# Optimization experiments

Hardware: AMD Instinct MI355X
Metric: run time of the kernel (lower is better)

## Reference

```python
import jax, jax.numpy as jnp
import numpy as np

H, HD, NKV = 16, 128, 4           # heads, head_dim, n_kv_heads (kv_groups=4)
SEL_TOPK, SEL_DIM, SEL_HEADS = 64, 64, 1
ROPE_BASE = 10000.0


def _rope_emb(t, hd):
    inv = 1.0 / (ROPE_BASE ** (jnp.arange(0, hd, 2, dtype=jnp.float32) / hd))
    freqs = jnp.arange(t, dtype=jnp.float32)[:, None] * inv[None, :]
    return jnp.concatenate([freqs, freqs], axis=-1)  # [t, hd]


def _apply_rotary(x, rope):
    # x: [b, t, h, hd]; rope: [t, hd] (rot_dim == hd here)
    cos = jnp.cos(rope)[None, :, None, :]
    sin = jnp.sin(rope)[None, :, None, :]
    x1, x2 = x[..., ::2], x[..., 1::2]
    c, s = cos[..., ::2], sin[..., ::2]
    rot = jnp.stack([x1 * c - x2 * s, x1 * s + x2 * c], axis=-1)
    return rot.reshape(x.shape)


def _selector_mask(q, k):
    # q, k: [b, H, t, hd] in UNrotated form (selector_rope='none'); causal=True
    b, h, t, d = q.shape
    qs = q[:, :SEL_HEADS, :, :SEL_DIM]
    ks = k[:, :SEL_HEADS, :, :SEL_DIM]
    scores = jnp.einsum('bhqd,bhkd->bhqk', qs, ks) / np.sqrt(SEL_DIM).astype(np.float32)
    future = jnp.triu(jnp.ones((t, t), bool), 1)
    scores = jnp.where(future[None, None], -jnp.inf, scores)
    idx = jax.lax.top_k(scores, SEL_TOPK)[1]  # [b, h_sel, t, keep]
    rows = jnp.arange(t)
    scatter_row = lambda im: jnp.zeros((t, t), bool).at[rows[:, None], im].set(True)
    sel = jax.vmap(jax.vmap(scatter_row))(idx)          # [b, h_sel, t, t]
    sel = sel.at[:, :, rows, rows].set(True)            # diagonal always kept
    sel = sel & jnp.tril(jnp.ones((t, t), bool))[None, None]
    sel = jnp.any(sel, axis=1, keepdims=True)           # h_sel < h -> broadcast mask
    return jnp.where(sel, 0.0, -jnp.inf).astype(jnp.float32)


def reference(x, Wq, bq, Wkd, bkd, Wku, bku, Wo, bo):
    b, t, d = x.shape
    G = H // NKV
    q = (x @ Wq + bq).reshape(b, t, H, HD)
    kv = (x @ Wkd + bkd) @ Wku + bku                    # MLA: down then up projection
    k = kv[..., : NKV * HD].reshape(b, t, NKV, HD)
    v = kv[..., NKV * HD:].reshape(b, t, NKV, HD)
    rope = _rope_emb(t, HD)
    qb = _apply_rotary(q, rope).transpose(0, 2, 1, 3)                     # [b,H,t,hd]
    kb = jnp.repeat(_apply_rotary(k, rope).transpose(0, 2, 1, 3), G, 1)   # GQA expand
    vb = jnp.repeat(v.transpose(0, 2, 1, 3), G, 1)
    # selector mask from unrotated q/k, detached (selector_detach=True)
    qu = jax.lax.stop_gradient(q.transpose(0, 2, 1, 3))
    ku = jnp.repeat(jax.lax.stop_gradient(k.transpose(0, 2, 1, 3)), G, 1)
    mask = _selector_mask(qu, ku)                                         # [b,1,t,t]
    scores = jnp.einsum('bhqd,bhkd->bhqk', qb, kb) / np.sqrt(HD).astype(np.float32)
    attn = jax.nn.softmax(scores + mask, axis=-1)
    y = jnp.einsum('bhqk,bhkd->bhqd', attn, vb)
    y = y.transpose(0, 2, 1, 3).reshape(b, t, H * HD)
    return y @ Wo + bo


def setup_inputs() -> dict:
    key = jax.random.key(0)
    ks = jax.random.split(key, 6)
    B, T, D, LAT = 2, 2048, 2048, 512
    s = 0.02
    return {
        'x': jax.random.normal(ks[0], (B, T, D), jnp.float32),
        'Wq': jax.random.normal(ks[1], (D, H * HD), jnp.float32) * s,
        'bq': jnp.zeros((H * HD,), jnp.float32),
        'Wkd': jax.random.normal(ks[2], (D, LAT), jnp.float32) * s,
        'bkd': jnp.zeros((LAT,), jnp.float32),
        'Wku': jax.random.normal(ks[3], (LAT, 2 * NKV * HD), jnp.float32) * s,
        'bku': jnp.zeros((2 * NKV * HD,), jnp.float32),
        'Wo': jax.random.normal(ks[4], (H * HD, D), jnp.float32) * s,
        'bo': jnp.zeros((D,), jnp.float32),
    }
```

## Files before the change

kernel.cpp:

```cpp
#include <hip/hip_runtime.h>

typedef unsigned int u32;
typedef unsigned long long u64;
typedef _Float16 f16;
typedef __attribute__((ext_vector_type(2))) _Float16 f16x2;
typedef __attribute__((ext_vector_type(4))) _Float16 f16x4;
typedef __attribute__((ext_vector_type(8))) _Float16 f16x8;
typedef __attribute__((ext_vector_type(4))) float f32x4;
typedef __attribute__((ext_vector_type(2))) double f64x2;


__device__ __forceinline__ int suX(int jj) { return jj ^ ((jj >> 4) & 7); }

__device__ __forceinline__ void dev_transpose_cast(char* smem, int bx, int by,
                                                   const float* __restrict__ in,
                                                   f16* __restrict__ out, int R, int C)
{
  float* tile = (float*)smem;
  int c0 = bx * 32, r0 = by * 32;
  int tx = threadIdx.x & 31, ty = threadIdx.x >> 5;
  #pragma unroll
  for (int i = ty; i < 32; i += 8) tile[i * 33 + tx] = in[(size_t)(r0 + i) * C + c0 + tx];
  __syncthreads();
  #pragma unroll
  for (int i = ty; i < 32; i += 8) out[(size_t)(c0 + i) * R + r0 + tx] = (f16)tile[tx * 33 + i];
}

__global__ __launch_bounds__(256) void k_megaP(const float* __restrict__ Wq, f16* __restrict__ WqT,
                                               const float* __restrict__ Wkd, f16* __restrict__ WkdT,
                                               const float* __restrict__ Wku, f16* __restrict__ WkuT,
                                               const float* __restrict__ Wo, f16* __restrict__ WoT,
                                               const float* __restrict__ x, f16* __restrict__ xh,
                                               double* __restrict__ Bsel,
                                               const float* __restrict__ bq,
                                               const float* __restrict__ bkd,
                                               const float* __restrict__ bku,
                                               double* __restrict__ bsel,
                                               float* __restrict__ rc, float* __restrict__ rs)
{
  __shared__ __align__(16) char smem[4224];
  const int id = blockIdx.x;
  const int tid = threadIdx.x;
  if (id < 4096) {
    dev_transpose_cast(smem, id & 63, id >> 6, Wq, WqT, 2048, 2048);
  } else if (id < 5120) {
    int g = id - 4096;
    dev_transpose_cast(smem, g & 15, g >> 4, Wkd, WkdT, 2048, 512);
  } else if (id < 5632) {
    int g = id - 5120;
    dev_transpose_cast(smem, g & 31, g >> 5, Wku, WkuT, 512, 1024);
  } else if (id < 9728) {
    int g = id - 5632;
    dev_transpose_cast(smem, g & 63, g >> 6, Wo, WoT, 2048, 2048);
  } else if (id < 17920) {
    int i = (id - 9728) * 256 + tid;
    f32x4 v = *(const f32x4*)&x[(size_t)i * 4];
    f16x4 h; h.x = (f16)v.x; h.y = (f16)v.y; h.z = (f16)v.z; h.w = (f16)v.w;
    *(f16x4*)&xh[(size_t)i * 4] = h;
  } else if (id < 18432) {
    const int k = (id - 17920) * 4 + (tid >> 6);
    const int j = tid & 63;
    Bsel[(size_t)k * 128 + j] = (double)Wq[(size_t)k * 2048 + j];
    double s = 0.0;
    for (int l = 0; l < 512; ++l)
      s = fma((double)Wkd[(size_t)k * 512 + l], (double)Wku[(size_t)l * 1024 + j], s);
    Bsel[(size_t)k * 128 + 64 + j] = s;
  } else if (id == 18432) {
    if (tid < 128) {
      int j = tid;
      if (j < 64) {
        bsel[j] = (double)bq[j];
      } else {
        int jj = j - 64;
        double s = (double)bku[jj];
        for (int l = 0; l < 512; ++l)
          s = fma((double)bkd[l], (double)Wku[(size_t)l * 1024 + jj], s);
        bsel[j] = s;
      }
    }
  } else {
    const int t = (id - 18433) * 4 + (tid >> 6);
    const int i = tid & 63;
    int fi = (2 * i) & 63;
    double inv = pow(10000.0, -(double)fi / 64.0);
    double a = (double)t * inv;
    rc[t * 64 + i] = (float)cos(a);
    rs[t * 64 + i] = (float)sin(a);
  }
}

__device__ __forceinline__ void dev_sel_f64(char* smem, int bx, int by, int bz,
                                            const float* __restrict__ A,
                                            const double* __restrict__ Bsel,
                                            double* __restrict__ partial)
{
  double* Asd = (double*)smem;
  double* Bsd = (double*)smem + 32 * 33;
  const int m0 = bx * 32, n0 = by * 64;
  const int kbase = bz * 256, kend = kbase + 256;
  const int tid = threadIdx.x;
  const int tx = tid & 15, ty = tid >> 4;
  const int ar = tid >> 3, ac4 = (tid & 7) * 4;
  double acc[2][4] = {};

  f32x4 aN = *(const f32x4*)&A[(size_t)(m0 + ar) * 2048 + kbase + ac4];
  f64x2 bN[4];
  #pragma unroll
  for (int it = 0; it < 4; ++it) {
    int c = it * 256 + tid; int kk = c >> 5, n2 = (c & 31) * 2;
    bN[it] = *(const f64x2*)&Bsel[(size_t)(kbase + kk) * 128 + n0 + n2];
  }
  for (int k0 = kbase; k0 < kend; k0 += 32) {
    __syncthreads();
    Asd[ar * 33 + ac4] = (double)aN.x; Asd[ar * 33 + ac4 + 1] = (double)aN.y;
    Asd[ar * 33 + ac4 + 2] = (double)aN.z; Asd[ar * 33 + ac4 + 3] = (double)aN.w;
    #pragma unroll
    for (int it = 0; it < 4; ++it) {
      int c = it * 256 + tid; int kk = c >> 5, n2 = (c & 31) * 2;
      Bsd[kk * 66 + n2] = bN[it].x; Bsd[kk * 66 + n2 + 1] = bN[it].y;
    }
    __syncthreads();
    if (k0 + 32 < kend) {
      aN = *(const f32x4*)&A[(size_t)(m0 + ar) * 2048 + k0 + 32 + ac4];
      #pragma unroll
      for (int it = 0; it < 4; ++it) {
        int c = it * 256 + tid; int kk = c >> 5, n2 = (c & 31) * 2;
        bN[it] = *(const f64x2*)&Bsel[(size_t)(k0 + 32 + kk) * 128 + n0 + n2];
      }
    }
    #pragma unroll
    for (int kk = 0; kk < 32; ++kk) {
      double a0 = Asd[(ty * 2) * 33 + kk], a1 = Asd[(ty * 2 + 1) * 33 + kk];
      f64x2 b01 = *(const f64x2*)&Bsd[kk * 66 + tx * 2];
      f64x2 b23 = *(const f64x2*)&Bsd[kk * 66 + tx * 2 + 32];
      acc[0][0] = fma(a0, b01.x, acc[0][0]); acc[0][1] = fma(a0, b01.y, acc[0][1]);
      acc[0][2] = fma(a0, b23.x, acc[0][2]); acc[0][3] = fma(a0, b23.y, acc[0][3]);
      acc[1][0] = fma(a1, b01.x, acc[1][0]); acc[1][1] = fma(a1, b01.y, acc[1][1]);
      acc[1][2] = fma(a1, b23.x, acc[1][2]); acc[1][3] = fma(a1, b23.y, acc[1][3]);
    }
  }
  double* op = partial + (size_t)bz * 4096 * 128;
  #pragma unroll
  for (int i = 0; i < 2; ++i) {
    int row = m0 + ty * 2 + i;
    #pragma unroll
    for (int j = 0; j < 2; ++j) {
      op[(size_t)row * 128 + n0 + tx * 2 + j] = acc[i][j];
      op[(size_t)row * 128 + n0 + tx * 2 + 32 + j] = acc[i][j + 2];
    }
  }
}

__device__ __forceinline__ void dev_sel_reduce(int blk,
                                               const double* __restrict__ partial,
                                               const double* __restrict__ bias,
                                               double* __restrict__ qs64,
                                               double* __restrict__ ks64)
{
  const int idx = blk * 256 + threadIdx.x;
  const int row = idx >> 7, n = idx & 127;
  const size_t S = 4096 * 128;
  double v = partial[idx];
  #pragma unroll
  for (int z = 1; z < 8; ++z) v += partial[(size_t)z * S + idx];
  v += bias[n];
  if (n < 64) qs64[(size_t)row * 64 + n] = v;
  else        ks64[(size_t)row * 64 + (n - 64)] = v;
}

__global__ __launch_bounds__(256) void k_transpose64(const double* __restrict__ in,
                                                     double* __restrict__ out)
{
  __shared__ double tile[32][33];
  const int bt = blockIdx.z;
  const int c0 = blockIdx.x * 32;
  const int r0 = blockIdx.y * 32;
  int tx = threadIdx.x & 31, ty = threadIdx.x >> 5;
  const double* ip = in + (size_t)bt * 2048 * 64;
  double* op = out + (size_t)bt * 64 * 2048;
  #pragma unroll
  for (int i = ty; i < 32; i += 8) tile[i][tx] = ip[(size_t)(r0 + i) * 64 + c0 + tx];
  __syncthreads();
  #pragma unroll
  for (int i = ty; i < 32; i += 8) op[(size_t)(c0 + i) * 2048 + r0 + tx] = tile[tx][i];
}

__device__ __forceinline__ void dev_score(char* smem, int sc,
                                          const double* __restrict__ qs,
                                          const double* __restrict__ ksT,
                                          u64* __restrict__ su)
{
  const int rt = sc >> 2;
  const int kc = sc & 3;
  const int tmax = ((rt & 127) << 4) + 15;
  if (kc * 512 > tmax) return;
  const int b = rt >> 7;
  const int tid = threadIdx.x;
  double* As = (double*)smem;
  {
    const double* qp = qs + (size_t)rt * 16 * 64;
    #pragma unroll
    for (int i = 0; i < 4; ++i) As[tid * 4 + i] = qp[tid * 4 + i];
  }
  __syncthreads();
  const int k0 = kc * 512 + tid;
  const int k1 = k0 + 256;
  const double* kb = ksT + (size_t)b * 64 * 2048;
  double acc0[16] = {}, acc1[16] = {};
  for (int d = 0; d < 64; ++d) {
    const double b0 = kb[(size_t)d * 2048 + k0];
    const double b1 = kb[(size_t)d * 2048 + k1];
    #pragma unroll
    for (int r = 0; r < 16; ++r) {
      const double a = As[r * 64 + d];
      acc0[r] = fma(a, b0, acc0[r]);
      acc1[r] = fma(a, b1, acc1[r]);
    }
  }
  #pragma unroll
  for (int r = 0; r < 16; ++r) {
    const int row = rt * 16 + r;
    u64 u0 = (u64)__double_as_longlong(acc0[r]);
    u0 = (u0 >> 63) ? ~u0 : (u0 | 0x8000000000000000ull);
    su[(size_t)row * 2048 + k0] = u0;
    u64 u1 = (u64)__double_as_longlong(acc1[r]);
    u1 = (u1 >> 63) ? ~u1 : (u1 | 0x8000000000000000ull);
    su[(size_t)row * 2048 + k1] = u1;
  }
}

template <int MODE>
__device__ __forceinline__ void dev_gemm_bt(char* smem, int gbx, int gby, int nbx, int nby,
                                            const f16* __restrict__ A,
                                            const f16* __restrict__ BT,
                                            const float* __restrict__ bias,
                                            float* __restrict__ C, f16* __restrict__ Ch,
                                            f16* __restrict__ Kout, f16* __restrict__ Vout,
                                            const float* __restrict__ rc,
                                            const float* __restrict__ rs,
                                            int K, int lda, int ldb, int ldc)
{
  f16* As = (f16*)smem;
  f16* Bs = (f16*)smem + 128 * 64;
  const int tid = threadIdx.x;
  const int lane = tid & 63;
  const int wave = tid >> 6;
  int bx = gbx, by = gby;
  {
    const int nwg = nbx * nby;
    if ((nwg & 7) == 0) {
      const int bid = by * nbx + bx;
      const int cpx = nwg >> 3;
      const int sbid = (bid & 7) * cpx + (bid >> 3);
      bx = sbid % nbx;
      by = sbid / nbx;
    }
  }
  const int m0 = bx * 128, n0 = by * 64;
  const int wr = (wave >> 1) * 64, wc = (wave & 1) * 32;
  const int lrow = lane & 15;
  const int kgrp = (lane >> 4) * 8;
  f32x4 acc[4][2] = {};

  for (int k0 = 0; k0 < K; k0 += 64) {
    __syncthreads();
    #pragma unroll
    for (int it = 0; it < 4; ++it) {
      int c = it * 256 + tid;
      int r = c >> 3, c8 = (c & 7) * 8;
      int lbase = (it * 256 + (tid & 192)) * 8;
      const f16* ga = A + (size_t)(m0 + r) * lda + k0 + c8;
      __builtin_amdgcn_global_load_lds((const __attribute__((address_space(1))) u32*)ga,
                                       (__attribute__((address_space(3))) u32*)&As[lbase],
                                       16, 0, 0);
    }
    #pragma unroll
    for (int it = 0; it < 2; ++it) {
      int c = it * 256 + tid;
      int r = c >> 3, c8 = (c & 7) * 8;
      int lbase = (it * 256 + (tid & 192)) * 8;
      const f16* gb = BT + (size_t)(n0 + r) * ldb + k0 + c8;
      __builtin_amdgcn_global_load_lds((const __attribute__((address_space(1))) u32*)gb,
                                       (__attribute__((address_space(3))) u32*)&Bs[lbase],
                                       16, 0, 0);
    }
    __syncthreads();
    #pragma unroll
    for (int ks = 0; ks < 2; ++ks) {
      f16x8 af[4], bfr[2];
      #pragma unroll
      for (int m = 0; m < 4; ++m)
        af[m] = *(const f16x8*)&As[(wr + m * 16 + lrow) * 64 + ks * 32 + kgrp];
      #pragma unroll
      for (int n = 0; n < 2; ++n)
        bfr[n] = *(const f16x8*)&Bs[(wc + n * 16 + lrow) * 64 + ks * 32 + kgrp];
      #pragma unroll
      for (int m = 0; m < 4; ++m)
        #pragma unroll
        for (int n = 0; n < 2; ++n)
          acc[m][n] = __builtin_amdgcn_mfma_f32_16x16x32_f16(af[m], bfr[n], acc[m][n], 0, 0, 0);
    }
  }
  const int rbase = m0 + wr + (lane >> 4) * 4;
  #pragma unroll
  for (int n = 0; n < 2; ++n) {
    int col = n0 + wc + n * 16 + lrow;
    float bv = bias ? bias[col] : 0.0f;
    const int ri = (col & 127) >> 1;
    #pragma unroll
    for (int m = 0; m < 4; ++m) {
      #pragma unroll
      for (int j = 0; j < 4; ++j) {
        int rowi = rbase + m * 16 + j;
        float v = acc[m][n][j] + bv;
        if (MODE == 0) {
          C[(size_t)rowi * ldc + col] = v;
        } else if (MODE == 1) {
          Ch[(size_t)rowi * ldc + col] = (f16)v;
        } else if (MODE == 2) {
          float vp = __shfl_xor(v, 1);
          int t = rowi & 2047;
          float c_ = rc[t * 64 + ri], s_ = rs[t * 64 + ri];
          float r_ = (lrow & 1) ? (vp * s_ + v * c_) : (v * c_ - vp * s_);
          Ch[(size_t)rowi * ldc + col] = (f16)r_;
        } else {
          float vp = __shfl_xor(v, 1);
          if (n0 < 512) {
            int t = rowi & 2047;
            float c_ = rc[t * 64 + ri], s_ = rs[t * 64 + ri];
            float r_ = (lrow & 1) ? (vp * s_ + v * c_) : (v * c_ - vp * s_);
            Kout[(size_t)rowi * 512 + col] = (f16)r_;
          } else {
            Vout[(size_t)rowi * 512 + (col - 512)] = (f16)v;
          }
        }
      }
    }
  }
}

__global__ __launch_bounds__(256) void k_fusedA(const float* __restrict__ x,
                                                const double* __restrict__ Bsel,
                                                double* __restrict__ partial,
                                                const f16* __restrict__ xh,
                                                const f16* __restrict__ WkdT,
                                                const float* __restrict__ bkd,
                                                f16* __restrict__ cbf)
{
  __shared__ __align__(16) char smem[25600];
  const int id = blockIdx.x;
  if (id < 2048) {
    dev_sel_f64(smem, id & 127, (id >> 7) & 1, id >> 8, x, Bsel, partial);
  } else {
    const int g = id - 2048;
    dev_gemm_bt<1>(smem, g & 31, g >> 5, 32, 8, xh, WkdT, bkd, nullptr, cbf,
                   nullptr, nullptr, nullptr, nullptr, 2048, 2048, 2048, 512);
  }
}

__global__ __launch_bounds__(256) void k_fusedC(const f16* __restrict__ cbf,
                                                const f16* __restrict__ WkuT,
                                                const float* __restrict__ bku,
                                                f16* __restrict__ krope, f16* __restrict__ vbf,
                                                const float* __restrict__ rc,
                                                const float* __restrict__ rs,
                                                const double* __restrict__ partial,
                                                const double* __restrict__ bsel,
                                                double* __restrict__ qs64,
                                                double* __restrict__ ks64)
{
  __shared__ __align__(16) char smem[24576];
  const int id = blockIdx.x;
  if (id < 512) {
    dev_gemm_bt<3>(smem, id & 31, id >> 5, 32, 16, cbf, WkuT, bku, nullptr, nullptr,
                   krope, vbf, rc, rs, 512, 512, 512, 1024);
  } else {
    dev_sel_reduce(id - 512, partial, bsel, qs64, ks64);
  }
}

__global__ __launch_bounds__(256) void k_fusedQS(const f16* __restrict__ xh,
                                                 const f16* __restrict__ WqT,
                                                 const float* __restrict__ bq,
                                                 f16* __restrict__ qrope,
                                                 const float* __restrict__ rc,
                                                 const float* __restrict__ rs,
                                                 const double* __restrict__ qs64,
                                                 const double* __restrict__ ksT,
                                                 u64* __restrict__ gsu)
{
  __shared__ __align__(16) char smem[24576];
  const int id = blockIdx.x;
  if (id < 1024) {
    dev_gemm_bt<2>(smem, id & 31, id >> 5, 32, 32, xh, WqT, bq, nullptr, qrope,
                   nullptr, nullptr, rc, rs, 2048, 2048, 2048, 2048);
  } else {
    dev_score(smem, id - 1024, qs64, ksT, gsu);
  }
}

__global__ __launch_bounds__(256) void k_gemmO(const f16* __restrict__ A,
                                               const f16* __restrict__ BT,
                                               const float* __restrict__ bias,
                                               float* __restrict__ C)
{
  __shared__ __align__(16) char smem[24576];
  dev_gemm_bt<0>(smem, blockIdx.x, blockIdx.y, 32, 32, A, BT, bias, C, nullptr,
                 nullptr, nullptr, nullptr, nullptr, 2048, 2048, 2048, 2048);
}

__global__ __launch_bounds__(256) void k_select(const u64* __restrict__ gsu,
                                                int* __restrict__ selcnt,
                                                int* __restrict__ selidx)
{
  const int row = blockIdx.x;
  const int t = row & 2047;
  const int tid = threadIdx.x;
  const int lane = tid & 63, wave = tid >> 6;
  int* outp = selidx + (size_t)row * 68;
  if (t < 64) {
    for (int jj = tid; jj <= t; jj += 256) outp[jj] = jj;
    if (tid == 0) selcnt[row] = t + 1;
    return;
  }
  __shared__ u64 su[2048];
  __shared__ unsigned hist[256];
  __shared__ unsigned wsum[4];
  __shared__ unsigned s_bsel, s_larger, s_cnt;
  __shared__ u64 s_thr;
  __shared__ int s_remfin;
  __shared__ int cand[128];
  __shared__ u64 ckey[128];

  {
    const u64* g = gsu + (size_t)row * 2048;
    for (int jj = tid; jj <= t; jj += 256) su[suX(jj)] = g[jj];
  }
  __syncthreads();

  const int c0 = tid * 8;
  u64 kv[8]; bool kvv[8];
  #pragma unroll
  for (int e = 0; e < 8; ++e) {
    const int jj = c0 + e;
    kvv[e] = (jj <= t);
    kv[e] = kvv[e] ? su[suX(jj)] : 0;
  }

  u64 prefix = 0;
  int remaining = 64;
  int broke = 0, sh_final = 0;
  for (int byte = 7; byte >= 0; --byte) {
    const int sh = byte * 8;
    hist[tid] = 0;
    __syncthreads();
    {
      unsigned bn[8]; bool vl[8];
      #pragma unroll
      for (int e = 0; e < 8; ++e) {
        vl[e] = kvv[e] && ((byte == 7) || (((kv[e] ^ prefix) >> (sh + 8)) == 0));
        bn[e] = (unsigned)((kv[e] >> sh) & 255);
      }
      unsigned myBin = 0xFFFFFFFFu, cntLoc = 0;
      bool localSame = true;
      #pragma unroll
      for (int e = 0; e < 8; ++e) {
        if (vl[e]) {
          if (myBin == 0xFFFFFFFFu) myBin = bn[e];
          else if (bn[e] != myBin) localSame = false;
          ++cntLoc;
        }
      }
      const bool hasValid = (cntLoc > 0);
      unsigned vmin = hasValid ? myBin : 0xFFFFFFFFu;
      unsigned vmax = hasValid ? myBin : 0u;
      unsigned csum = cntLoc;
      #pragma unroll
      for (int off = 32; off; off >>= 1) {
        unsigned a = __shfl_xor(vmin, off); vmin = a < vmin ? a : vmin;
        unsigned bmx = __shfl_xor(vmax, off); vmax = bmx > vmax ? bmx : vmax;
        csum += __shfl_xor(csum, off);
      }
      const bool anyMixed = (__ballot(hasValid && !localSame) != 0ull);
      const bool anyValid = (__ballot(hasValid) != 0ull);
      if (!anyMixed && anyValid && vmin == vmax) {
        if (lane == 0) atomicAdd(&hist[vmin], csum);
      } else if (hasValid) {
        #pragma unroll
        for (int e = 0; e < 8; ++e) {
          if (vl[e]) {
            bool first = true;
            #pragma unroll
            for (int p = 0; p < 8; ++p)
              if (p < e && vl[p] && bn[p] == bn[e]) first = false;
            if (first) {
              unsigned c = 0;
              #pragma unroll
              for (int q = 0; q < 8; ++q)
                if (q >= e && vl[q] && bn[q] == bn[e]) ++c;
              atomicAdd(&hist[bn[e]], c);
            }
          }
        }
      }
    }
    __syncthreads();
    const unsigned h = hist[tid];
    unsigned v = h;
    #pragma unroll
    for (int off = 1; off < 64; off <<= 1) {
      unsigned tv = __shfl_down(v, off);
      if (lane + off < 64) v += tv;
    }
    if (lane == 0) wsum[wave] = v;
    __syncthreads();
    unsigned add = 0;
    #pragma unroll
    for (int w = 0; w < 4; ++w)
      if (w > wave) add += wsum[w];
    const unsigned inc = v + add;
    const unsigned cumAbove = inc - h;
    __syncthreads();
    if ((int)cumAbove < remaining && (int)inc >= remaining) {
      s_bsel = (unsigned)tid;
      s_larger = cumAbove;
      s_cnt = inc - cumAbove;
    }
    __syncthreads();
    prefix |= ((u64)s_bsel << sh);
    remaining -= (int)s_larger;
    int cnt = (int)s_cnt;
    if (cnt <= 128) { broke = 1; sh_final = sh; break; }
  }
  u64 thr;
  int remfin;
  if (broke) {
    unsigned cg = 0;
    #pragma unroll
    for (int e = 0; e < 8; ++e)
      if (kvv[e] && (((kv[e] ^ prefix) >> sh_final) == 0)) ++cg;
    unsigned v = cg;
    #pragma unroll
    for (int off = 1; off < 64; off <<= 1) {
      unsigned tv = __shfl_up(v, off);
      if (lane >= off) v += tv;
    }
    __syncthreads();
    if (lane == 63) wsum[wave] = v;
    __syncthreads();
    unsigned add = 0, tot = 0;
    #pragma unroll
    for (int w = 0; w < 4; ++w) {
      tot += wsum[w];
      if (w < wave) add += wsum[w];
    }
    const int C = (int)tot;
    int pos = (int)(v + add - cg);
    __syncthreads();
    #pragma unroll
    for (int e = 0; e < 8; ++e)
      if (kvv[e] && (((kv[e] ^ prefix) >> sh_final) == 0)) cand[pos++] = c0 + e;
    __syncthreads();
    if (tid < C) ckey[tid] = su[suX(cand[tid])];
    __syncthreads();
    if (tid < C) {
      u64 k = ckey[tid];
      int g = 0, eq = 0;
      for (int j = 0; j < C; ++j) {
        g += (ckey[j] > k) ? 1 : 0;
        eq += (ckey[j] == k) ? 1 : 0;
      }
      if (g < remaining && remaining <= g + eq) {
        s_thr = k;
        s_remfin = remaining - g;
      }
    }
    __syncthreads();
    thr = s_thr;
    remfin = s_remfin;
  } else {
    thr = prefix;
    remfin = remaining;
  }
  __syncthreads();
  unsigned cg = 0, ct_ = 0;
  #pragma unroll
  for (int e = 0; e < 8; ++e) {
    if (kvv[e]) {
      cg += (kv[e] > thr) ? 1u : 0u;
      ct_ += (kv[e] == thr) ? 1u : 0u;
    }
  }
  const unsigned pack = cg | (ct_ << 16);
  {
    unsigned v = pack;
    #pragma unroll
    for (int off = 1; off < 64; off <<= 1) {
      unsigned tv = __shfl_up(v, off);
      if (lane >= off) v += tv;
    }
    if (lane == 63) wsum[wave] = v;
    __syncthreads();
    unsigned add = 0, tot = 0;
    #pragma unroll
    for (int w = 0; w < 4; ++w) {
      tot += wsum[w];
      if (w < wave) add += wsum[w];
    }
    const unsigned excl = v + add - pack;
    __syncthreads();
    const unsigned Gtot = tot & 0xFFFFu;
    const u64 ut = su[suX(t)];
    const unsigned gt = (ut > thr) ? 1u : 0u;
    const unsigned tt = (ut == thr) ? 1u : 0u;
    const int GtotX = (int)(Gtot - gt);
    int gpos = (int)(excl & 0xFFFFu);
    int tpos = (int)(excl >> 16);
    #pragma unroll
    for (int e = 0; e < 8; ++e) {
      const int jj = c0 + e;
      if (!kvv[e]) break;
      if (kv[e] > thr) {
        if (jj != t) outp[1 + gpos] = jj;
        ++gpos;
      } else if (kv[e] == thr) {
        if (jj != t && tpos < remfin) outp[1 + GtotX + tpos] = jj;
        ++tpos;
      }
    }
    if (tid == 0) {
      outp[0] = t;
      const unsigned Ttot = tot >> 16;
      int tb = (int)(Ttot - tt);
      int emitT = tb < remfin ? tb : remfin;
      selcnt[row] = 1 + GtotX + emitT;
    }
  }
}

__global__ __launch_bounds__(256) void k_attn(const f16* __restrict__ qr,
                                              const f16* __restrict__ kr,
                                              const f16* __restrict__ vv,
                                              const int* __restrict__ selcnt,
                                              const int* __restrict__ selidx,
                                              f16* __restrict__ y)
{
  const int blk = blockIdx.x;
  const int row = blk >> 2, kvh = blk & 3;
  const int b = row >> 11;
  const int tid = threadIdx.x, lane = tid & 63, wave = tid >> 6;
  const int cnt = selcnt[row];
  __shared__ int sidx[68];
  __shared__ __align__(16) f16 Kl[65 * 128];
  __shared__ __align__(16) f16 Vl[68 * 128];
  __shared__ __align__(4) f16 ph[4][72];
  if (tid < cnt) sidx[tid] = selidx[(size_t)row * 68 + tid];
  const f16* qb = qr + ((size_t)row * 16 + kvh * 4 + wave) * 128;
  f16x8 qf[16];
  #pragma unroll
  for (int i = 0; i < 16; ++i) qf[i] = *(const f16x8*)&qb[i * 8];
  __syncthreads();

  f16x8 kreg[5], vreg[5];
  int rr[5], cc[5]; bool vld[5];
  #pragma unroll
  for (int it = 0; it < 5; ++it) {
    const int c = it * 256 + tid;
    const int r = c >> 4, ch = c & 15;
    const bool ok = (r < cnt);
    const int rsafe = ok ? sidx[r] : sidx[0];
    const size_t kbase = ((size_t)(b * 2048 + rsafe)) * 512 + kvh * 128 + ch * 8;
    kreg[it] = *(const f16x8*)&kr[kbase];
    vreg[it] = *(const f16x8*)&vv[kbase];
    rr[it] = r; cc[it] = ch; vld[it] = ok;
  }
  #pragma unroll
  for (int it = 0; it < 5; ++it) {
    if (vld[it]) {
      *(f16x8*)&Kl[rr[it] * 128 + ((cc[it] ^ (rr[it] & 15)) * 8)] = kreg[it];
      *(f16x8*)&Vl[rr[it] * 128 + cc[it] * 8] = vreg[it];
    }
  }
  for (int i = tid; i < (68 - cnt) * 64; i += 256)
    ((u32*)Vl)[cnt * 64 + i] = 0u;
  __syncthreads();

  const float SCALE = 0.08838834764831845f;
  auto dotk = [&](int r) -> float {
    const int sw = r & 15;
    float s = 0.0f;
    #pragma unroll
    for (int i = 0; i < 16; ++i) {
      f16x8 k8 = *(const f16x8*)&Kl[r * 128 + ((i ^ sw) * 8)];
      f16x8 q8 = qf[i];
      #pragma unroll
      for (int e = 0; e < 4; ++e) {
        f16x2 ka; ka.x = k8[2 * e]; ka.y = k8[2 * e + 1];
        f16x2 qa; qa.x = q8[2 * e]; qa.y = q8[2 * e + 1];
        s = __builtin_amdgcn_fdot2(ka, qa, s, false);
      }
    }
    return s * SCALE;
  };

  float s1 = -__builtin_inff(), s2 = -__builtin_inff();
  if (lane < cnt) s1 = dotk(lane);
  if (lane + 64 < cnt) s2 = dotk(lane + 64);
  float mx = fmaxf(s1, s2);
  #pragma unroll
  for (int off = 32; off; off >>= 1) mx = fmaxf(mx, __shfl_xor(mx, off));
  float p1 = (lane < cnt) ? __expf(s1 - mx) : 0.0f;
  float p2 = (lane + 64 < cnt) ? __expf(s2 - mx) : 0.0f;
  float l = p1 + p2;
  #pragma unroll
  for (int off = 32; off; off >>= 1) l += __shfl_xor(l, off);
  float linv = 1.0f / l;
  ph[wave][lane] = (f16)p1;
  if (lane == 0) ph[wave][64] = (f16)p2;
  if (lane >= 1 && lane < 8) ph[wave][64 + lane] = (f16)0.f;
  __syncthreads();

  float y0 = 0.0f, y1 = 0.0f;
  const int d2 = lane * 2;
  for (int j = 0; j < cnt; j += 2) {
    f16x2 pp = *(const f16x2*)&ph[wave][j];
    f16x2 va = *(const f16x2*)&Vl[(j + 0) * 128 + d2];
    f16x2 vb = *(const f16x2*)&Vl[(j + 1) * 128 + d2];
    f16x2 v0; v0.x = va.x; v0.y = vb.x;
    f16x2 v1; v1.x = va.y; v1.y = vb.y;
    y0 = __builtin_amdgcn_fdot2(pp, v0, y0, false);
    y1 = __builtin_amdgcn_fdot2(pp, v1, y1, false);
  }
  y0 *= linv; y1 *= linv;
  f16x2 o; o.x = (f16)y0; o.y = (f16)y1;
  *(f16x2*)&y[(size_t)row * 2048 + (kvh * 4 + wave) * 128 + d2] = o;
}

extern "C" void kernel_launch(void* const* d_in, const int* in_sizes, int n_in,
                              void* d_out, int out_size, void* d_ws, size_t ws_size,
                              hipStream_t stream)
{
  (void)in_sizes; (void)n_in; (void)out_size; (void)ws_size;
  const float* x   = (const float*)d_in[0];
  const float* Wq  = (const float*)d_in[1];
  const float* bq  = (const float*)d_in[2];
  const float* Wkd = (const float*)d_in[3];
  const float* bkd = (const float*)d_in[4];
  const float* Wku = (const float*)d_in[5];
  const float* bku = (const float*)d_in[6];
  const float* Wo  = (const float*)d_in[7];
  const float* bo  = (const float*)d_in[8];
  float* out = (float*)d_out;

  char* ws = (char*)d_ws;
  size_t o = 0;
  auto alloc = [&](size_t bytes) -> void* {
    o = (o + 255) & ~(size_t)255;
    void* p = ws + o;
    o += bytes;
    return p;
  };
  f16* WqT   = (f16*)alloc(2048ull * 2048 * 2);
  f16* WoT   = (f16*)alloc(2048ull * 2048 * 2);
  f16* WkdT  = (f16*)alloc(512ull * 2048 * 2);
  f16* WkuT  = (f16*)alloc(1024ull * 512 * 2);
  f16* xh    = (f16*)alloc(4096ull * 2048 * 2);
  f16* yh    = (f16*)alloc(4096ull * 2048 * 2);
  f16* cbf   = (f16*)alloc(4096ull * 512 * 2);
  float* rc  = (float*)alloc(2048ull * 64 * 4);
  float* rs  = (float*)alloc(2048ull * 64 * 4);
  f16* qrope = (f16*)alloc(4096ull * 2048 * 2);
  f16* krope = (f16*)alloc(4096ull * 512 * 2);
  f16* vbf   = (f16*)alloc(4096ull * 512 * 2);
  int* selcnt = (int*)alloc(4096ull * 4);
  int* selidx = (int*)alloc(4096ull * 68 * 4);
  double* Bsel = (double*)alloc(2048ull * 128 * 8);
  double* bsel = (double*)alloc(128 * 8);
  double* qs64 = (double*)alloc(4096ull * 64 * 8);
  double* ks64 = (double*)alloc(4096ull * 64 * 8);
  double* ksT  = (double*)alloc(2ull * 64 * 2048 * 8);
  double* partial = (double*)alloc(8ull * 4096 * 128 * 8);
  u64* gsu = (u64*)alloc(4096ull * 2048 * 8);

  k_megaP<<<18945, 256, 0, stream>>>(Wq, WqT, Wkd, WkdT, Wku, WkuT, Wo, WoT, x, xh,
                                     Bsel, bq, bkd, bku, bsel, rc, rs);

  k_fusedA<<<2304, 256, 0, stream>>>(x, Bsel, partial, xh, WkdT, bkd, cbf);

  k_fusedC<<<2560, 256, 0, stream>>>(cbf, WkuT, bku, krope, vbf, rc, rs,
                                     partial, bsel, qs64, ks64);

  k_transpose64<<<dim3(2, 64, 2), 256, 0, stream>>>(ks64, ksT);

  k_fusedQS<<<2048, 256, 0, stream>>>(xh, WqT, bq, qrope, rc, rs, qs64, ksT, gsu);

  k_select<<<4096, 256, 0, stream>>>(gsu, selcnt, selidx);

  k_attn<<<16384, 256, 0, stream>>>(qrope, krope, vbf, selcnt, selidx, yh);

  k_gemmO<<<dim3(32, 32), 256, 0, stream>>>(yh, WoT, bo, out);
}
```

Baseline: 481.2 us.

## Split fused Q-GEMM/score kernel, enlarge score row tile, DMA score rows into LDS

```diff
diff --git a/kernel.cpp b/kernel.cpp
--- a/kernel.cpp
+++ b/kernel.cpp
@@ -9,8 +9,6 @@
 typedef __attribute__((ext_vector_type(4))) float f32x4;
 typedef __attribute__((ext_vector_type(2))) double f64x2;
 
-
-__device__ __forceinline__ int suX(int jj) { return jj ^ ((jj >> 4) & 7); }
 
 __device__ __forceinline__ void dev_transpose_cast(char* smem, int bx, int by,
                                                    const float* __restrict__ in,
@@ -185,41 +183,40 @@
   for (int i = ty; i < 32; i += 8) op[(size_t)(c0 + i) * 2048 + r0 + tx] = tile[tx][i];
 }
 
-__device__ __forceinline__ void dev_score(char* smem, int sc,
-                                          const double* __restrict__ qs,
-                                          const double* __restrict__ ksT,
-                                          u64* __restrict__ su)
-{
-  const int rt = sc >> 2;
-  const int kc = sc & 3;
-  const int tmax = ((rt & 127) << 4) + 15;
+__global__ __launch_bounds__(256) void k_score(const double* __restrict__ qs,
+                                               const double* __restrict__ ksT,
+                                               u64* __restrict__ su)
+{
+  const int rt = blockIdx.x >> 2;
+  const int kc = blockIdx.x & 3;
+  const int tmax = ((rt & 63) << 5) + 31;
   if (kc * 512 > tmax) return;
-  const int b = rt >> 7;
+  const int b = rt >> 6;
   const int tid = threadIdx.x;
-  double* As = (double*)smem;
+  __shared__ double As[32 * 64];
   {
-    const double* qp = qs + (size_t)rt * 16 * 64;
-    #pragma unroll
-    for (int i = 0; i < 4; ++i) As[tid * 4 + i] = qp[tid * 4 + i];
+    const double* qp = qs + (size_t)rt * 32 * 64;
+    #pragma unroll
+    for (int i = 0; i < 8; ++i) As[tid * 8 + i] = qp[tid * 8 + i];
   }
   __syncthreads();
   const int k0 = kc * 512 + tid;
   const int k1 = k0 + 256;
   const double* kb = ksT + (size_t)b * 64 * 2048;
-  double acc0[16] = {}, acc1[16] = {};
+  double acc0[32] = {}, acc1[32] = {};
   for (int d = 0; d < 64; ++d) {
     const double b0 = kb[(size_t)d * 2048 + k0];
     const double b1 = kb[(size_t)d * 2048 + k1];
     #pragma unroll
-    for (int r = 0; r < 16; ++r) {
+    for (int r = 0; r < 32; ++r) {
       const double a = As[r * 64 + d];
       acc0[r] = fma(a, b0, acc0[r]);
       acc1[r] = fma(a, b1, acc1[r]);
     }
   }
   #pragma unroll
-  for (int r = 0; r < 16; ++r) {
-    const int row = rt * 16 + r;
+  for (int r = 0; r < 32; ++r) {
+    const int row = rt * 32 + r;
     u64 u0 = (u64)__double_as_longlong(acc0[r]);
     u0 = (u0 >> 63) ? ~u0 : (u0 | 0x8000000000000000ull);
     su[(size_t)row * 2048 + k0] = u0;
@@ -379,24 +376,16 @@
   }
 }
 
-__global__ __launch_bounds__(256) void k_fusedQS(const f16* __restrict__ xh,
-                                                 const f16* __restrict__ WqT,
-                                                 const float* __restrict__ bq,
-                                                 f16* __restrict__ qrope,
-                                                 const float* __restrict__ rc,
-                                                 const float* __restrict__ rs,
-                                                 const double* __restrict__ qs64,
-                                                 const double* __restrict__ ksT,
-                                                 u64* __restrict__ gsu)
+__global__ __launch_bounds__(256) void k_gemmQ(const f16* __restrict__ xh,
+                                               const f16* __restrict__ WqT,
+                                               const float* __restrict__ bq,
+                                               f16* __restrict__ qrope,
+                                               const float* __restrict__ rc,
+                                               const float* __restrict__ rs)
 {
   __shared__ __align__(16) char smem[24576];
-  const int id = blockIdx.x;
-  if (id < 1024) {
-    dev_gemm_bt<2>(smem, id & 31, id >> 5, 32, 32, xh, WqT, bq, nullptr, qrope,
-                   nullptr, nullptr, rc, rs, 2048, 2048, 2048, 2048);
-  } else {
-    dev_score(smem, id - 1024, qs64, ksT, gsu);
-  }
+  dev_gemm_bt<2>(smem, blockIdx.x, blockIdx.y, 32, 32, xh, WqT, bq, nullptr, qrope,
+                 nullptr, nullptr, rc, rs, 2048, 2048, 2048, 2048);
 }
 
 __global__ __launch_bounds__(256) void k_gemmO(const f16* __restrict__ A,
@@ -423,7 +412,7 @@
     if (tid == 0) selcnt[row] = t + 1;
     return;
   }
-  __shared__ u64 su[2048];
+  __shared__ __align__(16) u64 su[2048];
   __shared__ unsigned hist[256];
   __shared__ unsigned wsum[4];
   __shared__ unsigned s_bsel, s_larger, s_cnt;
@@ -434,7 +423,14 @@
 
   {
     const u64* g = gsu + (size_t)row * 2048;
-    for (int jj = tid; jj <= t; jj += 256) su[suX(jj)] = g[jj];
+    #pragma unroll
+    for (int it = 0; it < 4; ++it) {
+      const u64* gp = g + (size_t)(it * 256 + tid) * 2;
+      __builtin_amdgcn_global_load_lds(
+          (const __attribute__((address_space(1))) u32*)gp,
+          (__attribute__((address_space(3))) u32*)&su[(size_t)(it * 256 + (tid & 192)) * 2],
+          16, 0, 0);
+    }
   }
   __syncthreads();
 
@@ -444,7 +440,7 @@
   for (int e = 0; e < 8; ++e) {
     const int jj = c0 + e;
     kvv[e] = (jj <= t);
-    kv[e] = kvv[e] ? su[suX(jj)] : 0;
+    kv[e] = kvv[e] ? su[jj] : 0;
   }
 
   u64 prefix = 0;
@@ -561,7 +557,7 @@
     for (int e = 0; e < 8; ++e)
       if (kvv[e] && (((kv[e] ^ prefix) >> sh_final) == 0)) cand[pos++] = c0 + e;
     __syncthreads();
-    if (tid < C) ckey[tid] = su[suX(cand[tid])];
+    if (tid < C) ckey[tid] = su[cand[tid]];
     __syncthreads();
     if (tid < C) {
       u64 k = ckey[tid];
@@ -610,7 +606,7 @@
     const unsigned excl = v + add - pack;
     __syncthreads();
     const unsigned Gtot = tot & 0xFFFFu;
-    const u64 ut = su[suX(t)];
+    const u64 ut = su[t];
     const unsigned gt = (ut > thr) ? 1u : 0u;
     const unsigned tt = (ut == thr) ? 1u : 0u;
     const int GtotX = (int)(Gtot - gt);
@@ -792,7 +788,8 @@
 
   k_transpose64<<<dim3(2, 64, 2), 256, 0, stream>>>(ks64, ksT);
 
-  k_fusedQS<<<2048, 256, 0, stream>>>(xh, WqT, bq, qrope, rc, rs, qs64, ksT, gsu);
+  k_gemmQ<<<dim3(32, 32), 256, 0, stream>>>(xh, WqT, bq, qrope, rc, rs);
+  k_score<<<512, 256, 0, stream>>>(qs64, ksT, gsu);
 
   k_select<<<4096, 256, 0, stream>>>(gsu, selcnt, selidx);
 
```

Result: no change. 481.2 us (median of 2 runs) (-0.0%).
